# Performance work log

Measured on AMD Instinct MI355X. Metric: run time of the kernel, lower is better.

Reference implementation:

```python
import jax, jax.numpy as jnp
import numpy as np

N_NODES = 100000
N_EDGES = 1600000
D = 128
L = 3


def setup_inputs() -> dict:
    key = jax.random.key(0)
    ks = jax.random.split(key, 5)
    x = jax.random.normal(ks[0], (N_NODES, D), dtype=jnp.float32)
    # Xavier-ish scale for stability through 3 layers
    scale = 1.0 / np.sqrt(D)
    W_self = jax.random.normal(ks[1], (L, D, D), dtype=jnp.float32) * scale
    W_neigh = jax.random.normal(ks[2], (L, D, D), dtype=jnp.float32) * scale
    bias = jnp.zeros((L, D), dtype=jnp.float32)
    src = jax.random.randint(ks[3], (N_EDGES,), 0, N_NODES)
    dst = jax.random.randint(ks[4], (N_EDGES,), 0, N_NODES)
    return {"x": x, "W_self": W_self, "W_neigh": W_neigh, "bias": bias,
            "src": src, "dst": dst}


def reference(x, W_self, W_neigh, bias, src, dst):
    """HomoSAGEEncoder forward (inference mode, dropout = identity).

    Each layer: DGL SAGEConv('mean'):
        h_neigh[v] = mean_{u in in-neighbors(v)} h[u]   (0 if no neighbors)
        h = h @ W_self + h_neigh @ W_neigh + bias
    followed by ReLU.
    """
    N = x.shape[0]
    n_layers = W_self.shape[0]
    # in-degree per destination node (shared across layers)
    deg = jax.ops.segment_sum(jnp.ones_like(dst, dtype=x.dtype), dst,
                              num_segments=N)
    inv_deg = (1.0 / jnp.maximum(deg, 1.0))[:, None]  # [N,1]

    h = x
    for l in range(n_layers):
        msg = h[src]  # [E,D] gather
        h_neigh = jax.ops.segment_sum(msg, dst, num_segments=N) * inv_deg
        h = h @ W_self[l] + h_neigh @ W_neigh[l] + bias[l]
        h = jax.nn.relu(h)
        # dropout is identity at inference; skipped
    return h
```

## Files before the change

### kernel.cpp

```cpp
#include <hip/hip_runtime.h>

typedef __attribute__((ext_vector_type(8))) short short8;
typedef __attribute__((ext_vector_type(4))) float f32x4;

static constexpr int NN = 100000;
static constexpr int NE = 1600000;
static constexpr int DD = 128;
static constexpr int NBUCK = 196;
static constexpr int CAP = 9216;

static constexpr int OFF_GCUR = 0;
static constexpr int OFF_OFFS = 512;
static constexpr int OFF_INV  = 100516;
static constexpr int OFF_WT   = 200520;
static constexpr int OFF_SS   = 249680;
static constexpr int OFF_HB   = 1849680;
static constexpr int OFF_HNB  = 8249680;

__device__ inline ushort f2b(float f) {
  uint u = __builtin_bit_cast(uint, f);
  uint r = (u + 0x7fffu + ((u >> 16) & 1u)) >> 16;
  return (ushort)r;
}
__device__ inline float b2f(ushort b) {
  uint u = ((uint)b) << 16;
  return __builtin_bit_cast(float, u);
}

__global__ __launch_bounds__(256) void k_pre(const float* __restrict__ x,
                                             const float* __restrict__ Ws,
                                             const float* __restrict__ Wn,
                                             ushort* __restrict__ hb,
                                             ushort* __restrict__ WtP,
                                             int* __restrict__ gcur) {
  int b = blockIdx.x, t = threadIdx.x;
  if (b < 12500) {
    int i = b * 256 + t;
    float4 v = *(const float4*)(x + (size_t)i * 4);
    uint2 p;
    p.x = (uint)f2b(v.x) | ((uint)f2b(v.y) << 16);
    p.y = (uint)f2b(v.z) | ((uint)f2b(v.w) << 16);
    *(uint2*)(hb + (size_t)i * 4) = p;
  } else if (b < 12884) {
    int i = (b - 12500) * 256 + t;
    int j = i & 7;
    int kg = (i >> 3) & 3;
    int col = (i >> 5) & 127;
    int kt = (i >> 12) & 7;
    int l = i >> 15;
    int k = kt * 32 + kg * 8 + j;
    float v = (k < 128) ? Ws[((size_t)l * 128 + k) * 128 + col]
                        : Wn[((size_t)l * 128 + (k - 128)) * 128 + col];
    WtP[i] = f2b(v);
  } else {
    gcur[t] = 0;
  }
}

__global__ __launch_bounds__(512) void k_bucket(const int* __restrict__ src,
                                                const int* __restrict__ dst,
                                                int* __restrict__ gcur,
                                                int* __restrict__ ebuf) {
  __shared__ int cnt[2][NBUCK];
  __shared__ int base[NBUCK];
  int t = threadIdx.x;
  int b0 = blockIdx.x * 4096;
  int half = t & 1;
  if (t < NBUCK) { cnt[0][t] = 0; cnt[1][t] = 0; }
  __syncthreads();
  int dv[8], pv[8];
#pragma unroll
  for (int j = 0; j < 8; ++j) {
    int idx = b0 + j * 512 + t;
    if (idx < NE) {
      int d = dst[idx];
      dv[j] = d;
      pv[j] = atomicAdd(&cnt[half][d >> 9], 1);
    } else dv[j] = -1;
  }
  __syncthreads();
  if (t < NBUCK) base[t] = atomicAdd(&gcur[t], cnt[0][t] + cnt[1][t]);
  __syncthreads();
#pragma unroll
  for (int j = 0; j < 8; ++j) {
    if (dv[j] >= 0) {
      int idx = b0 + j * 512 + t;
      int b = dv[j] >> 9;
      int pos = pv[j] + (half ? cnt[0][b] : 0);
      ebuf[(size_t)b * CAP + base[b] + pos] = ((dv[j] & 511) << 17) | src[idx];
    }
  }
}

__global__ __launch_bounds__(512) void k_sort(const int* __restrict__ ebuf,
                                              const int* __restrict__ gcur,
                                              int* __restrict__ offs,
                                              float* __restrict__ inv,
                                              int* __restrict__ ss) {
  __shared__ int cnt[512];
  __shared__ int sbase[512];
  __shared__ int scan[256];
  __shared__ int sarr[CAP];
  int b = blockIdx.x, t = threadIdx.x;
  if (t < 256) {
    int gv = (t < NBUCK) ? gcur[t] : 0;
    scan[t] = gv;
  }
  __syncthreads();
  for (int off = 1; off < 256; off <<= 1) {
    int u = (t < 256 && t >= off) ? scan[t - off] : 0;
    __syncthreads();
    if (t < 256) scan[t] += u;
    __syncthreads();
  }
  int nB = gcur[b];
  int base0 = scan[b] - nB;
  int n = nB;
  cnt[t] = 0;
  __syncthreads();
  const int* eb = ebuf + (size_t)b * CAP;
  for (int i = t; i < n; i += 512) atomicAdd(&cnt[(eb[i] >> 17) & 511], 1);
  __syncthreads();
  int c0 = 0, c1 = 0, s = 0;
  if (t < 256) {
    c0 = cnt[2 * t]; c1 = cnt[2 * t + 1];
    s = c0 + c1;
    scan[t] = s;
  }
  __syncthreads();
  for (int off = 1; off < 256; off <<= 1) {
    int u = (t < 256 && t >= off) ? scan[t - off] : 0;
    __syncthreads();
    if (t < 256) scan[t] += u;
    __syncthreads();
  }
  if (t < 256) {
    int eb2 = scan[t] - s;
    sbase[2 * t] = eb2;
    sbase[2 * t + 1] = eb2 + c0;
    int g0 = b * 512 + 2 * t, g1 = g0 + 1;
    if (g0 < NN) {
      offs[g0] = base0 + eb2;
      inv[g0] = 1.0f / (float)(c0 > 1 ? c0 : 1);
    }
    if (g1 < NN) {
      offs[g1] = base0 + eb2 + c0;
      inv[g1] = 1.0f / (float)(c1 > 1 ? c1 : 1);
    }
  }
  if (b == NBUCK - 1 && t == 0) offs[NN] = NE;
  __syncthreads();
  cnt[t] = 0;
  __syncthreads();
  for (int i = t; i < n; i += 512) {
    int e = eb[i];
    int ln = (e >> 17) & 511;
    int p = sbase[ln] + atomicAdd(&cnt[ln], 1);
    sarr[p] = e & 131071;
  }
  __syncthreads();
  for (int i = t; i < n; i += 512) ss[base0 + i] = sarr[i];
}

__global__ __launch_bounds__(256) void k_agg3(const ushort* __restrict__ h,
                                              const int* __restrict__ offs,
                                              const int* __restrict__ ss,
                                              const float* __restrict__ inv_deg,
                                              ushort* __restrict__ hN) {
  int gid = blockIdx.x * blockDim.x + threadIdx.x;
  int wid = gid >> 6;
  int lane = threadIdx.x & 63;
  int q = lane >> 4, l16 = lane & 15;
  int v = wid * 4 + q;
  int beg = offs[v], end = offs[v + 1];
  float a0 = 0, a1 = 0, a2 = 0, a3 = 0, a4 = 0, a5 = 0, a6 = 0, a7 = 0;
  const ushort* hp = h + (size_t)l16 * 8;
#define ACC8(u) { a0 += b2f((ushort)u.x); a1 += b2f((ushort)(u.x >> 16)); \
                  a2 += b2f((ushort)u.y); a3 += b2f((ushort)(u.y >> 16)); \
                  a4 += b2f((ushort)u.z); a5 += b2f((ushort)(u.z >> 16)); \
                  a6 += b2f((ushort)u.w); a7 += b2f((ushort)(u.w >> 16)); }
  int e = beg;
  for (; e + 7 < end; e += 8) {
    uint4 u0 = *(const uint4*)(hp + (size_t)ss[e + 0] * DD);
    uint4 u1 = *(const uint4*)(hp + (size_t)ss[e + 1] * DD);
    uint4 u2 = *(const uint4*)(hp + (size_t)ss[e + 2] * DD);
    uint4 u3 = *(const uint4*)(hp + (size_t)ss[e + 3] * DD);
    uint4 u4 = *(const uint4*)(hp + (size_t)ss[e + 4] * DD);
    uint4 u5 = *(const uint4*)(hp + (size_t)ss[e + 5] * DD);
    uint4 u6 = *(const uint4*)(hp + (size_t)ss[e + 6] * DD);
    uint4 u7 = *(const uint4*)(hp + (size_t)ss[e + 7] * DD);
    ACC8(u0) ACC8(u1) ACC8(u2) ACC8(u3) ACC8(u4) ACC8(u5) ACC8(u6) ACC8(u7)
  }
  for (; e < end; ++e) {
    uint4 u0 = *(const uint4*)(hp + (size_t)ss[e] * DD);
    ACC8(u0)
  }
#undef ACC8
  float w = inv_deg[v];
  a0 *= w; a1 *= w; a2 *= w; a3 *= w; a4 *= w; a5 *= w; a6 *= w; a7 *= w;
  uint4 p;
  p.x = (uint)f2b(a0) | ((uint)f2b(a1) << 16);
  p.y = (uint)f2b(a2) | ((uint)f2b(a3) << 16);
  p.z = (uint)f2b(a4) | ((uint)f2b(a5) << 16);
  p.w = (uint)f2b(a6) | ((uint)f2b(a7) << 16);
  *(uint4*)(hN + (size_t)v * DD + l16 * 8) = p;
}

__global__ __launch_bounds__(256) void k_gemm3(
    const ushort* __restrict__ hA, const ushort* __restrict__ hNb,
    const ushort* __restrict__ WtP, const float* __restrict__ bias,
    ushort* __restrict__ hOutB, float* __restrict__ outF, int writeF) {
  int w = threadIdx.x >> 6;
  int lane = threadIdx.x & 63;
  int r = lane & 15, kg = lane >> 4;
  int colbase = w * 32;
  int row0 = blockIdx.x * 32;

  short8 bfrag[8][2];
#pragma unroll
  for (int kt = 0; kt < 8; ++kt)
#pragma unroll
    for (int nt = 0; nt < 2; ++nt) {
      int col = colbase + nt * 16 + r;
      bfrag[kt][nt] = *(const short8*)(WtP + ((size_t)(kt * 128 + col) * 4 + kg) * 8);
    }
  float bv[2];
  bv[0] = bias[colbase + r];
  bv[1] = bias[colbase + 16 + r];

  int ra0 = row0 + r;
  int ra1 = row0 + 16 + r;

  f32x4 acc[2][2];
#pragma unroll
  for (int mt = 0; mt < 2; ++mt)
#pragma unroll
    for (int nt = 0; nt < 2; ++nt) acc[mt][nt] = (f32x4)0.f;

#pragma unroll
  for (int kt = 0; kt < 8; ++kt) {
    const ushort* hs = (kt < 4) ? hA : hNb;
    int kk = (kt & 3) * 32 + kg * 8;
    short8 a0 = *(const short8*)(hs + (size_t)ra0 * DD + kk);
    short8 a1 = *(const short8*)(hs + (size_t)ra1 * DD + kk);
    acc[0][0] = __builtin_amdgcn_mfma_f32_16x16x32_bf16(a0, bfrag[kt][0], acc[0][0], 0, 0, 0);
    acc[0][1] = __builtin_amdgcn_mfma_f32_16x16x32_bf16(a0, bfrag[kt][1], acc[0][1], 0, 0, 0);
    acc[1][0] = __builtin_amdgcn_mfma_f32_16x16x32_bf16(a1, bfrag[kt][0], acc[1][0], 0, 0, 0);
    acc[1][1] = __builtin_amdgcn_mfma_f32_16x16x32_bf16(a1, bfrag[kt][1], acc[1][1], 0, 0, 0);
  }

  __syncthreads();

#pragma unroll
  for (int mt = 0; mt < 2; ++mt) {
#pragma unroll
    for (int j = 0; j < 4; ++j) {
      int row = row0 + mt * 16 + kg * 4 + j;
#pragma unroll
      for (int nt = 0; nt < 2; ++nt) {
        float val = fmaxf(acc[mt][nt][j] + bv[nt], 0.f);
        int col = colbase + nt * 16 + r;
        if (writeF) outF[(size_t)row * DD + col] = val;
        else        hOutB[(size_t)row * DD + col] = f2b(val);
      }
    }
  }
}

extern "C" void kernel_launch(void* const* d_in, const int* in_sizes, int n_in,
                              void* d_out, int out_size, void* d_ws, size_t ws_size,
                              hipStream_t stream) {
  const float* x    = (const float*)d_in[0];
  const float* Ws   = (const float*)d_in[1];
  const float* Wn   = (const float*)d_in[2];
  const float* bias = (const float*)d_in[3];
  const int*   src  = (const int*)d_in[4];
  const int*   dst  = (const int*)d_in[5];
  float* out = (float*)d_out;

  int* ws      = (int*)d_ws;
  int* gcur    = ws + OFF_GCUR;
  int* offs    = ws + OFF_OFFS;
  float* inv   = (float*)(ws + OFF_INV);
  ushort* WtP  = (ushort*)(ws + OFF_WT);
  int* ssorted = ws + OFF_SS;
  ushort* hB   = (ushort*)(ws + OFF_HB);
  ushort* hNb  = (ushort*)(ws + OFF_HNB);
  int* ebuf    = ws + OFF_HNB;

  k_pre<<<12885, 256, 0, stream>>>(x, Ws, Wn, hB, WtP, gcur);
  k_bucket<<<(NE + 4095) / 4096, 512, 0, stream>>>(src, dst, gcur, ebuf);
  k_sort<<<NBUCK, 512, 0, stream>>>(ebuf, gcur, offs, inv, ssorted);

  for (int l = 0; l < 3; ++l) {
    k_agg3<<<NN / 16, 256, 0, stream>>>(hB, offs, ssorted, inv, hNb);
    k_gemm3<<<NN / 32, 256, 0, stream>>>(
        hB, hNb, WtP + (size_t)l * 8 * 128 * 32, bias + l * DD, hB, out, l == 2 ? 1 : 0);
  }
}
```

Measured before the change: 505.5 us.

## Use finer 128-node buckets with separate bucket prefix-scan kernel for CSR build

Splits the destination range into 784 buckets of 128 nodes instead of 196 buckets of 512, so the local sort runs across more blocks with smaller shared-memory arrays and 256 threads each. The bucket-offset prefix scan, previously repeated redundantly in every sort block, moves into a dedicated single-block kernel that writes bucket bases to the workspace. This is meant to raise occupancy and parallelism in the sort phase at the cost of one extra kernel launch and more global atomics in the bucketing step. Per-bucket capacity drops to 2560, which relies on the uniform random degree distribution not overflowing a bucket.

Result: no change. 512.9 us (+1.5%).

```diff
diff --git a/kernel.cpp b/kernel.cpp
--- a/kernel.cpp
+++ b/kernel.cpp
@@ -6,16 +6,17 @@
 static constexpr int NN = 100000;
 static constexpr int NE = 1600000;
 static constexpr int DD = 128;
-static constexpr int NBUCK = 196;
-static constexpr int CAP = 9216;
-
-static constexpr int OFF_GCUR = 0;
-static constexpr int OFF_OFFS = 512;
-static constexpr int OFF_INV  = 100516;
-static constexpr int OFF_WT   = 200520;
-static constexpr int OFF_SS   = 249680;
-static constexpr int OFF_HB   = 1849680;
-static constexpr int OFF_HNB  = 8249680;
+static constexpr int NBUCK = 784;
+static constexpr int CAP = 2560;
+
+static constexpr int OFF_GCUR  = 0;
+static constexpr int OFF_BBASE = 1024;
+static constexpr int OFF_OFFS  = 2048;
+static constexpr int OFF_INV   = 102052;
+static constexpr int OFF_WT    = 202056;
+static constexpr int OFF_SS    = 251208;
+static constexpr int OFF_HB    = 1851216;
+static constexpr int OFF_HNB   = 8251216;
 
 __device__ inline ushort f2b(float f) {
   uint u = __builtin_bit_cast(uint, f);
@@ -53,7 +54,8 @@
                         : Wn[((size_t)l * 128 + (k - 128)) * 128 + col];
     WtP[i] = f2b(v);
   } else {
-    gcur[t] = 0;
+    int i = (b - 12884) * 256 + t;
+    if (i < NBUCK) gcur[i] = 0;
   }
 }
 
@@ -66,7 +68,7 @@
   int t = threadIdx.x;
   int b0 = blockIdx.x * 4096;
   int half = t & 1;
-  if (t < NBUCK) { cnt[0][t] = 0; cnt[1][t] = 0; }
+  for (int i = t; i < NBUCK; i += 512) { cnt[0][i] = 0; cnt[1][i] = 0; }
   __syncthreads();
   int dv[8], pv[8];
 #pragma unroll
@@ -75,91 +77,90 @@
     if (idx < NE) {
       int d = dst[idx];
       dv[j] = d;
-      pv[j] = atomicAdd(&cnt[half][d >> 9], 1);
+      pv[j] = atomicAdd(&cnt[half][d >> 7], 1);
     } else dv[j] = -1;
   }
   __syncthreads();
-  if (t < NBUCK) base[t] = atomicAdd(&gcur[t], cnt[0][t] + cnt[1][t]);
+  for (int i = t; i < NBUCK; i += 512)
+    base[i] = atomicAdd(&gcur[i], cnt[0][i] + cnt[1][i]);
   __syncthreads();
 #pragma unroll
   for (int j = 0; j < 8; ++j) {
     if (dv[j] >= 0) {
       int idx = b0 + j * 512 + t;
-      int b = dv[j] >> 9;
+      int b = dv[j] >> 7;
       int pos = pv[j] + (half ? cnt[0][b] : 0);
-      ebuf[(size_t)b * CAP + base[b] + pos] = ((dv[j] & 511) << 17) | src[idx];
+      ebuf[(size_t)b * CAP + base[b] + pos] = ((dv[j] & 127) << 17) | src[idx];
     }
   }
 }
 
-__global__ __launch_bounds__(512) void k_sort(const int* __restrict__ ebuf,
-                                              const int* __restrict__ gcur,
+__global__ __launch_bounds__(512) void k_bscan(const int* __restrict__ gcur,
+                                               int* __restrict__ bbase) {
+  __shared__ int sc[1024];
+  int t = threadIdx.x;
+  int v0 = (t < NBUCK) ? gcur[t] : 0;
+  int v1 = (t + 512 < NBUCK) ? gcur[t + 512] : 0;
+  sc[t] = v0; sc[t + 512] = v1;
+  __syncthreads();
+  for (int off = 1; off < 1024; off <<= 1) {
+    int a0 = (t >= off) ? sc[t - off] : 0;
+    int a1 = (t + 512 >= off) ? sc[t + 512 - off] : 0;
+    __syncthreads();
+    sc[t] += a0; sc[t + 512] += a1;
+    __syncthreads();
+  }
+  if (t < NBUCK) bbase[t] = sc[t] - v0;
+  if (t + 512 < NBUCK) bbase[t + 512] = sc[t + 512] - v1;
+  if (t == 0) bbase[NBUCK] = NE;
+}
+
+__global__ __launch_bounds__(256) void k_sort(const int* __restrict__ ebuf,
+                                              const int* __restrict__ bbase,
                                               int* __restrict__ offs,
                                               float* __restrict__ inv,
                                               int* __restrict__ ss) {
-  __shared__ int cnt[512];
-  __shared__ int sbase[512];
-  __shared__ int scan[256];
+  __shared__ int cnt[128];
+  __shared__ int sbase[128];
+  __shared__ int scan[128];
   __shared__ int sarr[CAP];
   int b = blockIdx.x, t = threadIdx.x;
-  if (t < 256) {
-    int gv = (t < NBUCK) ? gcur[t] : 0;
-    scan[t] = gv;
-  }
-  __syncthreads();
-  for (int off = 1; off < 256; off <<= 1) {
-    int u = (t < 256 && t >= off) ? scan[t - off] : 0;
+  int base0 = bbase[b];
+  int n = bbase[b + 1] - base0;
+  if (t < 128) cnt[t] = 0;
+  __syncthreads();
+  const int* eb = ebuf + (size_t)b * CAP;
+  for (int i = t; i < n; i += 256) atomicAdd(&cnt[(eb[i] >> 17) & 127], 1);
+  __syncthreads();
+  int s = 0;
+  if (t < 128) { s = cnt[t]; scan[t] = s; }
+  __syncthreads();
+  for (int off = 1; off < 128; off <<= 1) {
+    int u = (t < 128 && t >= off) ? scan[t - off] : 0;
     __syncthreads();
-    if (t < 256) scan[t] += u;
+    if (t < 128) scan[t] += u;
     __syncthreads();
   }
-  int nB = gcur[b];
-  int base0 = scan[b] - nB;
-  int n = nB;
-  cnt[t] = 0;
-  __syncthreads();
-  const int* eb = ebuf + (size_t)b * CAP;
-  for (int i = t; i < n; i += 512) atomicAdd(&cnt[(eb[i] >> 17) & 511], 1);
-  __syncthreads();
-  int c0 = 0, c1 = 0, s = 0;
-  if (t < 256) {
-    c0 = cnt[2 * t]; c1 = cnt[2 * t + 1];
-    s = c0 + c1;
-    scan[t] = s;
-  }
-  __syncthreads();
-  for (int off = 1; off < 256; off <<= 1) {
-    int u = (t < 256 && t >= off) ? scan[t - off] : 0;
-    __syncthreads();
-    if (t < 256) scan[t] += u;
-    __syncthreads();
-  }
-  if (t < 256) {
+  if (t < 128) {
     int eb2 = scan[t] - s;
-    sbase[2 * t] = eb2;
-    sbase[2 * t + 1] = eb2 + c0;
-    int g0 = b * 512 + 2 * t, g1 = g0 + 1;
-    if (g0 < NN) {
-      offs[g0] = base0 + eb2;
-      inv[g0] = 1.0f / (float)(c0 > 1 ? c0 : 1);
+    sbase[t] = eb2;
+    int g = b * 128 + t;
+    if (g < NN) {
+      offs[g] = base0 + eb2;
+      inv[g] = 1.0f / (float)(s > 1 ? s : 1);
     }
-    if (g1 < NN) {
-      offs[g1] = base0 + eb2 + c0;
-      inv[g1] = 1.0f / (float)(c1 > 1 ? c1 : 1);
-    }
+    cnt[t] = 0;
   }
   if (b == NBUCK - 1 && t == 0) offs[NN] = NE;
   __syncthreads();
-  cnt[t] = 0;
-  __syncthreads();
-  for (int i = t; i < n; i += 512) {
+  for (int i = t; i < n; i += 256) {
     int e = eb[i];
-    int ln = (e >> 17) & 511;
+    int ln = (e >> 17) & 127;
     int p = sbase[ln] + atomicAdd(&cnt[ln], 1);
     sarr[p] = e & 131071;
   }
   __syncthreads();
-  for (int i = t; i < n; i += 512) ss[base0 + i] = sarr[i];
+  for (int i = t; i < n; i += 256) ss[base0 + i] = sarr[i];
 }
 
 __global__ __launch_bounds__(256) void k_agg3(const ushort* __restrict__ h,
@@ -280,6 +281,7 @@
 
   int* ws      = (int*)d_ws;
   int* gcur    = ws + OFF_GCUR;
+  int* bbase   = ws + OFF_BBASE;
   int* offs    = ws + OFF_OFFS;
   float* inv   = (float*)(ws + OFF_INV);
   ushort* WtP  = (ushort*)(ws + OFF_WT);
@@ -288,9 +290,10 @@
   ushort* hNb  = (ushort*)(ws + OFF_HNB);
   int* ebuf    = ws + OFF_HNB;
 
-  k_pre<<<12885, 256, 0, stream>>>(x, Ws, Wn, hB, WtP, gcur);
+  k_pre<<<12888, 256, 0, stream>>>(x, Ws, Wn, hB, WtP, gcur);
   k_bucket<<<(NE + 4095) / 4096, 512, 0, stream>>>(src, dst, gcur, ebuf);
-  k_sort<<<NBUCK, 512, 0, stream>>>(ebuf, gcur, offs, inv, ssorted);
+  k_bscan<<<1, 512, 0, stream>>>(gcur, bbase);
+  k_sort<<<NBUCK, 256, 0, stream>>>(ebuf, bbase, offs, inv, ssorted);
 
   for (int l = 0; l < 3; ++l) {
     k_agg3<<<NN / 16, 256, 0, stream>>>(hB, offs, ssorted, inv, hNb);
```
